# Performance work log

Measured on AMD Instinct MI355X. Metric: run time of the kernel, lower is better.

## Reference

```python
import jax, jax.numpy as jnp
import numpy as np


def _cdist(x, y):
    # x: (b, n, c), y: (b, m, c) -> (b, n, m) Euclidean distances
    x2 = jnp.sum(x * x, axis=-1, keepdims=True)          # (b, n, 1)
    y2 = jnp.sum(y * y, axis=-1)[:, None, :]             # (b, 1, m)
    xy = jnp.einsum('bnc,bmc->bnm', x, y)                # (b, n, m)
    d2 = jnp.maximum(x2 + y2 - 2.0 * xy, 0.0)
    return jnp.sqrt(d2)


def setup_inputs() -> dict:
    key = jax.random.key(0)
    k1, k2, k3, k4 = jax.random.split(key, 4)
    bs, N, M, C = 8, 4096, 4096, 128
    return {
        'set1': jax.random.normal(k1, (bs, N, C), dtype=jnp.float32),
        'set2': jax.random.normal(k2, (bs, M, C), dtype=jnp.float32),
        'w1': jax.random.uniform(k3, (bs, N), dtype=jnp.float32),
        'w2': jax.random.uniform(k4, (bs, M), dtype=jnp.float32),
    }


def reference(set1, set2, w1, w2):
    dist = _cdist(set1, set2)                 # (b, N, M)
    out_dist = jnp.min(dist, axis=2)          # (b, N)
    out_dist2 = jnp.min(dist, axis=1)         # (b, M)
    total = (jnp.sum(w1 * out_dist) + jnp.sum(w2 * out_dist2)) / 2.0
    return total
```

## Files before the change

### kernel.cpp

```cpp
#include <hip/hip_runtime.h>

#define BS 8
#define NN 4096
#define MM 4096
#define CC 128
#define XT 128
#define YT 128
#define MH 1024
#define NMT (MH / YT)
#define NXT (NN / XT)
#define SLICE (YT * 64)

#define FINF_BITS 0x7F800000u

typedef __attribute__((ext_vector_type(8))) short bf16x8;
typedef __attribute__((ext_vector_type(4))) float f32x4;

#define WAITVn(n) asm volatile("s_waitcnt vmcnt(" #n ")" ::: "memory")
#define SCHED_FENCE() __builtin_amdgcn_sched_barrier(0)

__device__ inline ushort f2bf(float f) {
    unsigned u = __float_as_uint(f);
    unsigned r = (u + 0x7FFFu + ((u >> 16) & 1u)) >> 16;
    return (ushort)r;
}

__global__ void ch_prep(const float* __restrict__ y,
                        ushort* __restrict__ y16, float* __restrict__ yn,
                        unsigned* __restrict__ rowmin, unsigned* __restrict__ colmin,
                        float* __restrict__ out) {
    int gid = blockIdx.x * blockDim.x + threadIdx.x;
    size_t i = (size_t)gid * 8;

    float4 w0 = *(const float4*)(y + i);
    float4 w1 = *(const float4*)(y + i + 4);
    ushort h[8] = {f2bf(w0.x), f2bf(w0.y), f2bf(w0.z), f2bf(w0.w),
                   f2bf(w1.x), f2bf(w1.y), f2bf(w1.z), f2bf(w1.w)};
    *(bf16x8*)(y16 + i) = *(bf16x8*)h;
    float sy = w0.x * w0.x + w0.y * w0.y + w0.z * w0.z + w0.w * w0.w +
               w1.x * w1.x + w1.y * w1.y + w1.z * w1.z + w1.w * w1.w;

#pragma unroll
    for (int mask = 1; mask <= 8; mask <<= 1)
        sy += __shfl_xor(sy, mask, 64);
    if ((threadIdx.x & 15) == 0)
        yn[gid >> 4] = sy;

    if (gid < BS * NN) rowmin[gid] = FINF_BITS;
    if (gid < BS * MM) colmin[gid] = FINF_BITS;
    if (gid == 0) out[0] = 0.0f;
}

__device__ __forceinline__ void stage_y(const ushort* __restrict__ Yb,
                                        ushort* __restrict__ buf,
                                        int tile, int half, int tid, int wave) {
#pragma unroll
    for (int s = 0; s < 4; ++s) {
        int f = s * 256 + tid;
        int r = f >> 3, cslot = f & 7;
        const ushort* g = Yb + (size_t)(tile * YT + r) * CC + half * 64 +
                          ((cslot ^ (r & 7)) * 8);
        ushort* l = buf + (size_t)(s * 256 + wave * 64) * 8;
        __builtin_amdgcn_global_load_lds(
            (const __attribute__((address_space(1))) void*)g,
            (__attribute__((address_space(3))) void*)l, 16, 0, 0);
    }
}

__global__ __launch_bounds__(256, 2) void ch_tile(
    const float* __restrict__ Xf, const ushort* __restrict__ Y,
    const float* __restrict__ yn,
    unsigned* __restrict__ rowmin, unsigned* __restrict__ colmin) {

    __shared__ ushort pool[4 * SLICE];
    __shared__ unsigned coltile[MH];
    __shared__ unsigned rowtile[XT];
    __shared__ float xnorm[XT];
    __shared__ float ynld[MH];

    const int b  = blockIdx.x;
    const int xt = blockIdx.y;
    const int mh = blockIdx.z;
    const int n0 = xt * XT;
    const int m0 = mh * MH;
    const int tid  = threadIdx.x;
    const int lane = tid & 63;
    const int wave = tid >> 6;
    const int lc   = lane & 15;
    const int quad = lane >> 4;
    const int wm = wave >> 1;
    const int wn = wave & 1;

    const ushort* Yb = Y + ((size_t)b * MM + m0) * CC;

    ushort* xs = pool;
    const float* Xb = Xf + ((size_t)b * NN + n0) * CC;
    {
        float psum[8];
#pragma unroll
        for (int s = 0; s < 8; ++s) {
            int flat = s * 256 + tid;
            int r = flat >> 4, c = flat & 15;
            float4 v0 = *(const float4*)(Xb + (size_t)r * CC + c * 8);
            float4 v1 = *(const float4*)(Xb + (size_t)r * CC + c * 8 + 4);
            ushort h[8] = {f2bf(v0.x), f2bf(v0.y), f2bf(v0.z), f2bf(v0.w),
                           f2bf(v1.x), f2bf(v1.y), f2bf(v1.z), f2bf(v1.w)};
            *(bf16x8*)(xs + r * CC + (c ^ (r & 7)) * 8) = *(bf16x8*)h;
            psum[s] = v0.x * v0.x + v0.y * v0.y + v0.z * v0.z + v0.w * v0.w +
                      v1.x * v1.x + v1.y * v1.y + v1.z * v1.z + v1.w * v1.w;
        }
#pragma unroll
        for (int mask = 1; mask <= 8; mask <<= 1)
#pragma unroll
            for (int s = 0; s < 8; ++s)
                psum[s] += __shfl_xor(psum[s], mask, 64);
        if ((tid & 15) == 0) {
#pragma unroll
            for (int s = 0; s < 8; ++s)
                xnorm[s * 16 + (tid >> 4)] = psum[s];
        }
    }
    {
        const float* ynb = yn + (size_t)b * MM + m0;
#pragma unroll
        for (int s = 0; s < MH / 256; ++s)
            ynld[s * 256 + tid] = ynb[s * 256 + tid];
    }
    for (int c2 = tid; c2 < MH; c2 += 256) coltile[c2] = FINF_BITS;
    if (tid < XT) rowtile[tid] = FINF_BITS;

    __syncthreads();

    bf16x8 af[4][4];
    const int xrow = (wm * 64 + lc) * CC;
    const int xsw  = lc & 7;
#pragma unroll
    for (int kt = 0; kt < 4; ++kt)
#pragma unroll
        for (int i = 0; i < 4; ++i)
            af[kt][i] = *(const bf16x8*)(xs + xrow + i * 16 * CC +
                                         ((kt * 4 + quad) ^ xsw) * 8);

    float xnp[4][4];
#pragma unroll
    for (int i = 0; i < 4; ++i) {
        float4 t = *(const float4*)(&xnorm[wm * 64 + i * 16 + quad * 4]);
        xnp[i][0] = t.x; xnp[i][1] = t.y; xnp[i][2] = t.z; xnp[i][3] = t.w;
    }
    float rm[4][4];
#pragma unroll
    for (int i = 0; i < 4; ++i)
#pragma unroll
        for (int r = 0; r < 4; ++r) rm[i][r] = __builtin_inff();

    __syncthreads();

    stage_y(Yb, pool + 0 * SLICE, 0, 0, tid, wave);
    stage_y(Yb, pool + 1 * SLICE, 0, 1, tid, wave);
    WAITVn(0);
    __builtin_amdgcn_s_barrier();
    SCHED_FENCE();

    const f32x4 z = {0.f, 0.f, 0.f, 0.f};

#pragma unroll 1
    for (int t = 0; t < NMT; ++t) {
        const ushort* ybase = pool + (t & 1) * (2 * SLICE);

        if (t + 1 < NMT) {
            ushort* wbase = pool + ((t + 1) & 1) * (2 * SLICE);
            stage_y(Yb, wbase, t + 1, 0, tid, wave);
            stage_y(Yb, wbase + SLICE, t + 1, 1, tid, wave);
        }

        float ynr[4];
#pragma unroll
        for (int j = 0; j < 4; ++j)
            ynr[j] = ynld[t * YT + wn * 64 + j * 16 + lc];

        f32x4 acc[4][4];
#pragma unroll
        for (int h = 0; h < 2; ++h) {
            const ushort* ybuf = ybase + h * SLICE;
#pragma unroll
            for (int s2 = 0; s2 < 2; ++s2) {
                const int ktg = h * 2 + s2;
                bf16x8 yf[4];
                const int cy = ((s2 * 4 + quad) ^ xsw) * 8;
#pragma unroll
                for (int j = 0; j < 4; ++j)
                    yf[j] = *(const bf16x8*)(ybuf + (wn * 64 + j * 16 + lc) * 64 + cy);
                __builtin_amdgcn_s_setprio(1);
#pragma unroll
                for (int j = 0; j < 4; ++j)
#pragma unroll
                    for (int i = 0; i < 4; ++i)
                        acc[i][j] = __builtin_amdgcn_mfma_f32_16x16x32_bf16(
                            af[ktg][i], yf[j], (ktg == 0) ? z : acc[i][j], 0, 0, 0);
                __builtin_amdgcn_s_setprio(0);
            }
        }

        float cmv[4];
#pragma unroll
        for (int j = 0; j < 4; ++j) cmv[j] = __builtin_inff();
#pragma unroll
        for (int i = 0; i < 4; ++i) {
#pragma unroll
            for (int j = 0; j < 4; ++j) {
                f32x4 a = acc[i][j];
                float e[4];
#pragma unroll
                for (int r = 0; r < 4; ++r)
                    e[r] = xnp[i][r] + fmaf(-2.0f, a[r], ynr[j]);
#pragma unroll
                for (int r = 0; r < 4; ++r)
                    rm[i][r] = fminf(rm[i][r], e[r]);
                cmv[j] = fminf(cmv[j],
                               fminf(fminf(e[0], e[1]), fminf(e[2], e[3])));
            }
        }
#pragma unroll
        for (int mask = 16; mask <= 32; mask <<= 1)
#pragma unroll
            for (int j = 0; j < 4; ++j)
                cmv[j] = fminf(cmv[j], __shfl_xor(cmv[j], mask, 64));
        if (quad == 0) {
#pragma unroll
            for (int j = 0; j < 4; ++j)
                atomicMin(&coltile[t * YT + wn * 64 + j * 16 + lc],
                          __float_as_uint(fmaxf(cmv[j], 0.0f)));
        }

        SCHED_FENCE();
        WAITVn(0);
        __builtin_amdgcn_s_barrier();
        SCHED_FENCE();
    }

#pragma unroll
    for (int mask = 1; mask <= 8; mask <<= 1)
#pragma unroll
        for (int i = 0; i < 4; ++i)
#pragma unroll
            for (int r = 0; r < 4; ++r)
                rm[i][r] = fminf(rm[i][r], __shfl_xor(rm[i][r], mask, 64));
    if (lc == 0) {
#pragma unroll
        for (int i = 0; i < 4; ++i)
#pragma unroll
            for (int r = 0; r < 4; ++r)
                atomicMin(&rowtile[wm * 64 + i * 16 + quad * 4 + r],
                          __float_as_uint(fmaxf(rm[i][r], 0.0f)));
    }

    __syncthreads();
    if (tid < XT)
        atomicMin(&rowmin[(size_t)b * NN + n0 + tid], rowtile[tid]);
    for (int c2 = tid; c2 < MH; c2 += 256)
        atomicMin(&colmin[(size_t)b * MM + m0 + c2], coltile[c2]);
}

__global__ void ch_finalize(const unsigned* __restrict__ rowmin,
                            const unsigned* __restrict__ colmin,
                            const float* __restrict__ w1,
                            const float* __restrict__ w2,
                            float* __restrict__ out) {
    int i = blockIdx.x * blockDim.x + threadIdx.x;
    int stride = gridDim.x * blockDim.x;
    float s = 0.f;
    for (int idx = i; idx < BS * NN; idx += stride)
        s += w1[idx] * sqrtf(__uint_as_float(rowmin[idx])) +
             w2[idx] * sqrtf(__uint_as_float(colmin[idx]));
#pragma unroll
    for (int off = 32; off > 0; off >>= 1) s += __shfl_down(s, off, 64);
    __shared__ float ls[4];
    int lane = threadIdx.x & 63, wv = threadIdx.x >> 6;
    if (lane == 0) ls[wv] = s;
    __syncthreads();
    if (threadIdx.x == 0) {
        float t = ls[0] + ls[1] + ls[2] + ls[3];
        atomicAdd(out, 0.5f * t);
    }
}

extern "C" void kernel_launch(void* const* d_in, const int* in_sizes, int n_in,
                              void* d_out, int out_size, void* d_ws, size_t ws_size,
                              hipStream_t stream) {
    const float* set1 = (const float*)d_in[0];
    const float* set2 = (const float*)d_in[1];
    const float* w1   = (const float*)d_in[2];
    const float* w2   = (const float*)d_in[3];
    float* out = (float*)d_out;

    ushort*   y16    = (ushort*)d_ws;
    float*    yn     = (float*)(y16 + (size_t)BS * MM * CC);
    unsigned* rowmin = (unsigned*)(yn + BS * MM);
    unsigned* colmin = rowmin + BS * NN;

    ch_prep<<<BS * MM * CC / 8 / 256, 256, 0, stream>>>(
        set2, y16, yn, rowmin, colmin, out);

    dim3 grid(BS, NXT, MM / MH);
    ch_tile<<<grid, 256, 0, stream>>>(set1, y16, yn, rowmin, colmin);

    ch_finalize<<<64, 256, 0, stream>>>(rowmin, colmin, w1, w2, out);
}
```

Before: 127.3 us.

## Stage Y per wave with a three-slot ring buffer and drop block barriers

```diff
diff --git a/kernel.cpp b/kernel.cpp
--- a/kernel.cpp
+++ b/kernel.cpp
@@ -6,10 +6,11 @@
 #define CC 128
 #define XT 128
 #define YT 128
-#define MH 1024
+#define MH 2048
 #define NMT (MH / YT)
+#define NPH (4 * NMT)
 #define NXT (NN / XT)
-#define SLICE (YT * 64)
+#define QS (64 * 32)
 
 #define FINF_BITS 0x7F800000u
 
@@ -51,16 +52,16 @@
     if (gid == 0) out[0] = 0.0f;
 }
 
-__device__ __forceinline__ void stage_y(const ushort* __restrict__ Yb,
-                                        ushort* __restrict__ buf,
-                                        int tile, int half, int tid, int wave) {
+__device__ __forceinline__ void stage_yw(const ushort* __restrict__ Yb,
+                                         ushort* __restrict__ buf,
+                                         int tile, int kt, int lane, int wn) {
 #pragma unroll
     for (int s = 0; s < 4; ++s) {
-        int f = s * 256 + tid;
-        int r = f >> 3, cslot = f & 7;
-        const ushort* g = Yb + (size_t)(tile * YT + r) * CC + half * 64 +
-                          ((cslot ^ (r & 7)) * 8);
-        ushort* l = buf + (size_t)(s * 256 + wave * 64) * 8;
+        int f = s * 64 + lane;
+        int r = f >> 2, cslot = f & 3;
+        const ushort* g = Yb + (size_t)(tile * YT + wn * 64 + r) * CC +
+                          kt * 32 + ((cslot ^ (r & 3)) * 8);
+        ushort* l = buf + (size_t)(s * 64) * 8;
         __builtin_amdgcn_global_load_lds(
             (const __attribute__((address_space(1))) void*)g,
             (__attribute__((address_space(3))) void*)l, 16, 0, 0);
@@ -72,7 +73,7 @@
     const float* __restrict__ yn,
     unsigned* __restrict__ rowmin, unsigned* __restrict__ colmin) {
 
-    __shared__ ushort pool[4 * SLICE];
+    __shared__ ushort pool[4 * 3 * QS];
     __shared__ unsigned coltile[MH];
     __shared__ unsigned rowtile[XT];
     __shared__ float xnorm[XT];
@@ -155,87 +156,85 @@
 
     __syncthreads();
 
-    stage_y(Yb, pool + 0 * SLICE, 0, 0, tid, wave);
-    stage_y(Yb, pool + 1 * SLICE, 0, 1, tid, wave);
-    WAITVn(0);
-    __builtin_amdgcn_s_barrier();
+    ushort* wslc = pool + wave * 3 * QS;
+    stage_yw(Yb, wslc + 0 * QS, 0, 0, lane, wn);
+    stage_yw(Yb, wslc + 1 * QS, 0, 1, lane, wn);
+    WAITVn(4);
     SCHED_FENCE();
 
     const f32x4 z = {0.f, 0.f, 0.f, 0.f};
+    int rdw = 0;
 
 #pragma unroll 1
     for (int t = 0; t < NMT; ++t) {
-        const ushort* ybase = pool + (t & 1) * (2 * SLICE);
-
-        if (t + 1 < NMT) {
-            ushort* wbase = pool + ((t + 1) & 1) * (2 * SLICE);
-            stage_y(Yb, wbase, t + 1, 0, tid, wave);
-            stage_y(Yb, wbase + SLICE, t + 1, 1, tid, wave);
-        }
-
+        f32x4 acc[4][4];
         float ynr[4];
 #pragma unroll
         for (int j = 0; j < 4; ++j)
             ynr[j] = ynld[t * YT + wn * 64 + j * 16 + lc];
 
-        f32x4 acc[4][4];
-#pragma unroll
-        for (int h = 0; h < 2; ++h) {
-            const ushort* ybuf = ybase + h * SLICE;
-#pragma unroll
-            for (int s2 = 0; s2 < 2; ++s2) {
-                const int ktg = h * 2 + s2;
-                bf16x8 yf[4];
-                const int cy = ((s2 * 4 + quad) ^ xsw) * 8;
-#pragma unroll
-                for (int j = 0; j < 4; ++j)
-                    yf[j] = *(const bf16x8*)(ybuf + (wn * 64 + j * 16 + lc) * 64 + cy);
-                __builtin_amdgcn_s_setprio(1);
-#pragma unroll
-                for (int j = 0; j < 4; ++j)
-#pragma unroll
-                    for (int i = 0; i < 4; ++i)
-                        acc[i][j] = __builtin_amdgcn_mfma_f32_16x16x32_bf16(
-                            af[ktg][i], yf[j], (ktg == 0) ? z : acc[i][j], 0, 0, 0);
-                __builtin_amdgcn_s_setprio(0);
+#pragma unroll
+        for (int kt = 0; kt < 4; ++kt) {
+            const int ph = 4 * t + kt;
+            if (ph + 2 < NPH) {
+                int wr = rdw + 2; if (wr >= 3) wr -= 3;
+                stage_yw(Yb, wslc + wr * QS, (ph + 2) >> 2, (ph + 2) & 3,
+                         lane, wn);
             }
+            const ushort* ybuf = wslc + rdw * QS;
+            const int cs = (quad ^ (lc & 3)) * 8;
+            bf16x8 yf[4];
+#pragma unroll
+            for (int j = 0; j < 4; ++j)
+                yf[j] = *(const bf16x8*)(ybuf + (j * 16 + lc) * 32 + cs);
+            __builtin_amdgcn_s_setprio(1);
+#pragma unroll
+            for (int j = 0; j < 4; ++j)
+#pragma unroll
+                for (int i = 0; i < 4; ++i)
+                    acc[i][j] = __builtin_amdgcn_mfma_f32_16x16x32_bf16(
+                        af[kt][i], yf[j], (kt == 0) ? z : acc[i][j], 0, 0, 0);
+            __builtin_amdgcn_s_setprio(0);
+
+            if (kt == 3) {
+                float cmv[4];
+#pragma unroll
+                for (int j = 0; j < 4; ++j) cmv[j] = __builtin_inff();
+#pragma unroll
+                for (int i = 0; i < 4; ++i) {
+#pragma unroll
+                    for (int j = 0; j < 4; ++j) {
+                        f32x4 a = acc[i][j];
+                        float e[4];
+#pragma unroll
+                        for (int r = 0; r < 4; ++r)
+                            e[r] = xnp[i][r] + fmaf(-2.0f, a[r], ynr[j]);
+#pragma unroll
+                        for (int r = 0; r < 4; ++r)
+                            rm[i][r] = fminf(rm[i][r], e[r]);
+                        cmv[j] = fminf(cmv[j],
+                                       fminf(fminf(e[0], e[1]),
+                                             fminf(e[2], e[3])));
+                    }
+                }
+#pragma unroll
+                for (int mask = 16; mask <= 32; mask <<= 1)
+#pragma unroll
+                    for (int j = 0; j < 4; ++j)
+                        cmv[j] = fminf(cmv[j], __shfl_xor(cmv[j], mask, 64));
+                if (quad == 0) {
+#pragma unroll
+                    for (int j = 0; j < 4; ++j)
+                        atomicMin(&coltile[t * YT + wn * 64 + j * 16 + lc],
+                                  __float_as_uint(fmaxf(cmv[j], 0.0f)));
+                }
+            }
+
+            SCHED_FENCE();
+            if (ph + 2 < NPH) { WAITVn(4); } else { WAITVn(0); }
+            SCHED_FENCE();
+            rdw = (rdw == 2) ? 0 : rdw + 1;
         }
-
-        float cmv[4];
-#pragma unroll
-        for (int j = 0; j < 4; ++j) cmv[j] = __builtin_inff();
-#pragma unroll
-        for (int i = 0; i < 4; ++i) {
-#pragma unroll
-            for (int j = 0; j < 4; ++j) {
-                f32x4 a = acc[i][j];
-                float e[4];
-#pragma unroll
-                for (int r = 0; r < 4; ++r)
-                    e[r] = xnp[i][r] + fmaf(-2.0f, a[r], ynr[j]);
-#pragma unroll
-                for (int r = 0; r < 4; ++r)
-                    rm[i][r] = fminf(rm[i][r], e[r]);
-                cmv[j] = fminf(cmv[j],
-                               fminf(fminf(e[0], e[1]), fminf(e[2], e[3])));
-            }
-        }
-#pragma unroll
-        for (int mask = 16; mask <= 32; mask <<= 1)
-#pragma unroll
-            for (int j = 0; j < 4; ++j)
-                cmv[j] = fminf(cmv[j], __shfl_xor(cmv[j], mask, 64));
-        if (quad == 0) {
-#pragma unroll
-            for (int j = 0; j < 4; ++j)
-                atomicMin(&coltile[t * YT + wn * 64 + j * 16 + lc],
-                          __float_as_uint(fmaxf(cmv[j], 0.0f)));
-        }
-
-        SCHED_FENCE();
-        WAITVn(0);
-        __builtin_amdgcn_s_barrier();
-        SCHED_FENCE();
     }
 
 #pragma unroll
```

Result: no change. 128.8 us (+1.2%).

## Halve LDS staging buffer to half-tile phases and raise occupancy to 3 blocks

Applied to the files above, without the earlier changes.

```diff
diff --git a/kernel.cpp b/kernel.cpp
--- a/kernel.cpp
+++ b/kernel.cpp
@@ -8,6 +8,7 @@
 #define YT 128
 #define MH 1024
 #define NMT (MH / YT)
+#define NPH (2 * NMT)
 #define NXT (NN / XT)
 #define SLICE (YT * 64)
 
@@ -16,7 +17,7 @@
 typedef __attribute__((ext_vector_type(8))) short bf16x8;
 typedef __attribute__((ext_vector_type(4))) float f32x4;
 
-#define WAITVn(n) asm volatile("s_waitcnt vmcnt(" #n ")" ::: "memory")
+#define WAITV0() asm volatile("s_waitcnt vmcnt(0)" ::: "memory")
 #define SCHED_FENCE() __builtin_amdgcn_sched_barrier(0)
 
 __device__ inline ushort f2bf(float f) {
@@ -51,28 +52,12 @@
     if (gid == 0) out[0] = 0.0f;
 }
 
-__device__ __forceinline__ void stage_y(const ushort* __restrict__ Yb,
-                                        ushort* __restrict__ buf,
-                                        int tile, int half, int tid, int wave) {
-#pragma unroll
-    for (int s = 0; s < 4; ++s) {
-        int f = s * 256 + tid;
-        int r = f >> 3, cslot = f & 7;
-        const ushort* g = Yb + (size_t)(tile * YT + r) * CC + half * 64 +
-                          ((cslot ^ (r & 7)) * 8);
-        ushort* l = buf + (size_t)(s * 256 + wave * 64) * 8;
-        __builtin_amdgcn_global_load_lds(
-            (const __attribute__((address_space(1))) void*)g,
-            (__attribute__((address_space(3))) void*)l, 16, 0, 0);
-    }
-}
-
-__global__ __launch_bounds__(256, 2) void ch_tile(
+__global__ __launch_bounds__(256, 3) void ch_tile(
     const float* __restrict__ Xf, const ushort* __restrict__ Y,
     const float* __restrict__ yn,
     unsigned* __restrict__ rowmin, unsigned* __restrict__ colmin) {
 
-    __shared__ ushort pool[4 * SLICE];
+    __shared__ ushort pool[2 * SLICE];
     __shared__ unsigned coltile[MH];
     __shared__ unsigned rowtile[XT];
     __shared__ float xnorm[XT];
@@ -141,12 +126,6 @@
             af[kt][i] = *(const bf16x8*)(xs + xrow + i * 16 * CC +
                                          ((kt * 4 + quad) ^ xsw) * 8);
 
-    float xnp[4][4];
-#pragma unroll
-    for (int i = 0; i < 4; ++i) {
-        float4 t = *(const float4*)(&xnorm[wm * 64 + i * 16 + quad * 4]);
-        xnp[i][0] = t.x; xnp[i][1] = t.y; xnp[i][2] = t.z; xnp[i][3] = t.w;
-    }
     float rm[4][4];
 #pragma unroll
     for (int i = 0; i < 4; ++i)
@@ -155,9 +134,17 @@
 
     __syncthreads();
 
-    stage_y(Yb, pool + 0 * SLICE, 0, 0, tid, wave);
-    stage_y(Yb, pool + 1 * SLICE, 0, 1, tid, wave);
-    WAITVn(0);
+    const int tr = tid >> 3;
+    const size_t poff = (size_t)tr * CC + (((tid & 7) ^ (tr & 7)) * 8);
+    const ushort* gbase = Yb + poff;
+    ushort* lbase = pool + (size_t)(wave * 64) * 8;
+
+#pragma unroll
+    for (int s = 0; s < 4; ++s)
+        __builtin_amdgcn_global_load_lds(
+            (const __attribute__((address_space(1))) void*)(gbase + s * 4096),
+            (__attribute__((address_space(3))) void*)(lbase + s * 2048), 16, 0, 0);
+    WAITV0();
     __builtin_amdgcn_s_barrier();
     SCHED_FENCE();
 
@@ -165,23 +152,32 @@
 
 #pragma unroll 1
     for (int t = 0; t < NMT; ++t) {
-        const ushort* ybase = pool + (t & 1) * (2 * SLICE);
-
-        if (t + 1 < NMT) {
-            ushort* wbase = pool + ((t + 1) & 1) * (2 * SLICE);
-            stage_y(Yb, wbase, t + 1, 0, tid, wave);
-            stage_y(Yb, wbase + SLICE, t + 1, 1, tid, wave);
-        }
-
+        f32x4 acc[4][4];
         float ynr[4];
-#pragma unroll
-        for (int j = 0; j < 4; ++j)
-            ynr[j] = ynld[t * YT + wn * 64 + j * 16 + lc];
-
-        f32x4 acc[4][4];
+
 #pragma unroll
         for (int h = 0; h < 2; ++h) {
-            const ushort* ybuf = ybase + h * SLICE;
+            const int ph = 2 * t + h;
+            const ushort* ybuf = pool + (ph & 1) * SLICE;
+
+            if (ph + 1 < NPH) {
+                const ushort* gs = gbase + (size_t)((ph + 1) >> 1) * (YT * CC) +
+                                   ((ph + 1) & 1) * 64;
+                ushort* ls = lbase + ((ph + 1) & 1) * SLICE;
+#pragma unroll
+                for (int s = 0; s < 4; ++s)
+                    __builtin_amdgcn_global_load_lds(
+                        (const __attribute__((address_space(1))) void*)(gs + s * 4096),
+                        (__attribute__((address_space(3))) void*)(ls + s * 2048),
+                        16, 0, 0);
+            }
+
+            if (h == 0) {
+#pragma unroll
+                for (int j = 0; j < 4; ++j)
+                    ynr[j] = ynld[t * YT + wn * 64 + j * 16 + lc];
+            }
+
 #pragma unroll
             for (int s2 = 0; s2 < 2; ++s2) {
                 const int ktg = h * 2 + s2;
@@ -190,52 +186,55 @@
 #pragma unroll
                 for (int j = 0; j < 4; ++j)
                     yf[j] = *(const bf16x8*)(ybuf + (wn * 64 + j * 16 + lc) * 64 + cy);
-                __builtin_amdgcn_s_setprio(1);
 #pragma unroll
                 for (int j = 0; j < 4; ++j)
 #pragma unroll
                     for (int i = 0; i < 4; ++i)
                         acc[i][j] = __builtin_amdgcn_mfma_f32_16x16x32_bf16(
                             af[ktg][i], yf[j], (ktg == 0) ? z : acc[i][j], 0, 0, 0);
-                __builtin_amdgcn_s_setprio(0);
             }
+
+            if (h == 1) {
+                float cmv[4];
+#pragma unroll
+                for (int j = 0; j < 4; ++j) cmv[j] = __builtin_inff();
+#pragma unroll
+                for (int i = 0; i < 4; ++i) {
+                    float4 xq = *(const float4*)(&xnorm[wm * 64 + i * 16 + quad * 4]);
+#pragma unroll
+                    for (int j = 0; j < 4; ++j) {
+                        f32x4 a = acc[i][j];
+                        float g0 = fmaf(-2.0f, a[0], ynr[j]);
+                        float g1 = fmaf(-2.0f, a[1], ynr[j]);
+                        float g2 = fmaf(-2.0f, a[2], ynr[j]);
+                        float g3 = fmaf(-2.0f, a[3], ynr[j]);
+                        rm[i][0] = fminf(rm[i][0], g0);
+                        rm[i][1] = fminf(rm[i][1], g1);
+                        rm[i][2] = fminf(rm[i][2], g2);
+                        rm[i][3] = fminf(rm[i][3], g3);
+                        float m01 = fminf(xq.x + g0, xq.y + g1);
+                        float m23 = fminf(xq.z + g2, xq.w + g3);
+                        cmv[j] = fminf(cmv[j], fminf(m01, m23));
+                    }
+                }
+#pragma unroll
+                for (int mask = 16; mask <= 32; mask <<= 1)
+#pragma unroll
+                    for (int j = 0; j < 4; ++j)
+                        cmv[j] = fminf(cmv[j], __shfl_xor(cmv[j], mask, 64));
+                if (quad == 0) {
+#pragma unroll
+                    for (int j = 0; j < 4; ++j)
+                        atomicMin(&coltile[t * YT + wn * 64 + j * 16 + lc],
+                                  __float_as_uint(fmaxf(cmv[j], 0.0f)));
+                }
+            }
+
+            SCHED_FENCE();
+            WAITV0();
+            __builtin_amdgcn_s_barrier();
+            SCHED_FENCE();
         }
-
-        float cmv[4];
-#pragma unroll
-        for (int j = 0; j < 4; ++j) cmv[j] = __builtin_inff();
-#pragma unroll
-        for (int i = 0; i < 4; ++i) {
-#pragma unroll
-            for (int j = 0; j < 4; ++j) {
-                f32x4 a = acc[i][j];
-                float e[4];
-#pragma unroll
-                for (int r = 0; r < 4; ++r)
-                    e[r] = xnp[i][r] + fmaf(-2.0f, a[r], ynr[j]);
-#pragma unroll
-                for (int r = 0; r < 4; ++r)
-                    rm[i][r] = fminf(rm[i][r], e[r]);
-                cmv[j] = fminf(cmv[j],
-                               fminf(fminf(e[0], e[1]), fminf(e[2], e[3])));
-            }
-        }
-#pragma unroll
-        for (int mask = 16; mask <= 32; mask <<= 1)
-#pragma unroll
-            for (int j = 0; j < 4; ++j)
-                cmv[j] = fminf(cmv[j], __shfl_xor(cmv[j], mask, 64));
-        if (quad == 0) {
-#pragma unroll
-            for (int j = 0; j < 4; ++j)
-                atomicMin(&coltile[t * YT + wn * 64 + j * 16 + lc],
-                          __float_as_uint(fmaxf(cmv[j], 0.0f)));
-        }
-
-        SCHED_FENCE();
-        WAITVn(0);
-        __builtin_amdgcn_s_barrier();
-        SCHED_FENCE();
     }
 
 #pragma unroll
@@ -247,11 +246,14 @@
                 rm[i][r] = fminf(rm[i][r], __shfl_xor(rm[i][r], mask, 64));
     if (lc == 0) {
 #pragma unroll
-        for (int i = 0; i < 4; ++i)
+        for (int i = 0; i < 4; ++i) {
+            float4 xq = *(const float4*)(&xnorm[wm * 64 + i * 16 + quad * 4]);
+            float xr[4] = {xq.x, xq.y, xq.z, xq.w};
 #pragma unroll
             for (int r = 0; r < 4; ++r)
                 atomicMin(&rowtile[wm * 64 + i * 16 + quad * 4 + r],
-                          __float_as_uint(fmaxf(rm[i][r], 0.0f)));
+                          __float_as_uint(fmaxf(rm[i][r] + xr[r], 0.0f)));
+        }
     }
 
     __syncthreads();
```

New measurement: 157.7 us. 1.24x slower.
